# Kernel optimization log

Hardware: AMD Instinct MI355X
Metric: run time of the kernel (lower is better)

## Reference

```python
import jax, jax.numpy as jnp
import numpy as np

D_MODEL = 1024
N_HEADS = 16
D_K = D_MODEL // N_HEADS
D_FF = 4096
B, S = 2, 2048
LN_EPS = 1e-5
NEG_INF = -1e30  # finite stand-in for -inf; first (all-masked) row is overwritten by zeros anyway


def layer_norm(x, g, b):
    mu = jnp.mean(x, axis=-1, keepdims=True)
    var = jnp.mean(jnp.square(x - mu), axis=-1, keepdims=True)
    return (x - mu) * jax.lax.rsqrt(var + LN_EPS) * g + b


def setup_inputs() -> dict:
    key = jax.random.key(0)
    ks = jax.random.split(key, 16)
    sd = 0.02
    inp = {
        "query": jax.random.normal(ks[0], (B, S, D_MODEL), jnp.float32),
        "key": jax.random.normal(ks[1], (B, S, D_MODEL), jnp.float32),
        "values": jax.random.normal(ks[2], (B, S, D_MODEL), jnp.float32),
        "Wq": jax.random.normal(ks[3], (D_MODEL, D_MODEL), jnp.float32) * sd,
        "bq": jnp.zeros((D_MODEL,), jnp.float32),
        "Wk": jax.random.normal(ks[4], (D_MODEL, D_MODEL), jnp.float32) * sd,
        "bk": jnp.zeros((D_MODEL,), jnp.float32),
        "Wv": jax.random.normal(ks[5], (D_MODEL, D_MODEL), jnp.float32) * sd,
        "bv": jnp.zeros((D_MODEL,), jnp.float32),
        "Wo": jax.random.normal(ks[6], (D_MODEL, D_MODEL), jnp.float32) * sd,
        "bo": jnp.zeros((D_MODEL,), jnp.float32),
        "ln1_g": jnp.ones((D_MODEL,), jnp.float32),
        "ln1_b": jnp.zeros((D_MODEL,), jnp.float32),
        "W1": jax.random.normal(ks[7], (D_MODEL, D_FF), jnp.float32) * sd,
        "b1": jnp.zeros((D_FF,), jnp.float32),
        "W2": jax.random.normal(ks[8], (D_FF, D_MODEL), jnp.float32) * sd,
        "b2": jnp.zeros((D_MODEL,), jnp.float32),
        "ln2_g": jnp.ones((D_MODEL,), jnp.float32),
        "ln2_b": jnp.zeros((D_MODEL,), jnp.float32),
        "mask": 0,
    }
    return inp


def reference(query, key, values, Wq, bq, Wk, bk, Wv, bv, Wo, bo,
              ln1_g, ln1_b, W1, b1, W2, b2, ln2_g, ln2_b, mask):
    b, s, d = query.shape
    # projections -> [B, H, S, d_k]
    q = (query @ Wq + bq).reshape(b, s, N_HEADS, D_K).transpose(0, 2, 1, 3)
    k = (key @ Wk + bk).reshape(b, s, N_HEADS, D_K).transpose(0, 2, 1, 3)
    v = (values @ Wv + bv).reshape(b, s, N_HEADS, D_K).transpose(0, 2, 1, 3)
    # scores [B, H, S, S]
    scores = jnp.einsum("bhqd,bhkd->bhqk", q, k) / jnp.sqrt(jnp.float32(D_K))
    # torch: triu(ones, k=mask)==0 -> allowed iff j < i + mask
    i = jnp.arange(s)[:, None]
    j = jnp.arange(s)[None, :]
    allowed = j < (i + mask)
    scores = jnp.where(allowed, scores, NEG_INF)
    attn = jax.nn.softmax(scores, axis=-1)
    if mask == 0:
        # zero-pad trick: first query row (fully masked) is replaced by zeros
        attn = attn.at[:, :, 0, :].set(0.0)
    ctx = jnp.einsum("bhqk,bhkd->bhqd", attn, v)
    ctx = ctx.transpose(0, 2, 1, 3).reshape(b, s, d)
    attn_out = ctx @ Wo + bo
    x = layer_norm(query + attn_out, ln1_g, ln1_b)
    ffn = jax.nn.relu(x @ W1 + b1) @ W2 + b2
    out = layer_norm(x + ffn, ln2_g, ln2_b)
    return out
```

## Files before the change

kernel.cpp:

```cpp
#include <hip/hip_runtime.h>


typedef __attribute__((ext_vector_type(8))) __bf16 bf16x8;
typedef __attribute__((ext_vector_type(4))) float f32x4;

struct alignas(8)  S4 { short x, y, z, w; };
struct alignas(16) F4 { float x, y, z, w; };
struct alignas(16) I4 { int x, y, z, w; };

static __device__ __forceinline__ short f2bf(float f) {
  unsigned u = __float_as_uint(f);
  u += 0x7fff + ((u >> 16) & 1);
  return (short)(u >> 16);
}

static __device__ __forceinline__ void store_out(float* p, float v) { *p = v; }
static __device__ __forceinline__ void store_out(short* p, float v) { *p = f2bf(v); }

#define GLL16(g, l)                                                         \
  __builtin_amdgcn_global_load_lds(                                         \
      (__attribute__((address_space(1))) void*)(g),                         \
      (__attribute__((address_space(3))) void*)(l), 16, 0, 0)

__global__ __launch_bounds__(256) void cvt_bf16_kernel(
    const float* __restrict__ i0, const float* __restrict__ i1,
    const float* __restrict__ i2, short* __restrict__ o0,
    short* __restrict__ o1, short* __restrict__ o2) {
  int z = blockIdx.y;
  const float* in = z == 0 ? i0 : (z == 1 ? i1 : i2);
  short* out = z == 0 ? o0 : (z == 1 ? o1 : o2);
  int i = (blockIdx.x * 256 + threadIdx.x) * 4;
  F4 v = *(const F4*)(in + i);
  S4 o = { f2bf(v.x), f2bf(v.y), f2bf(v.z), f2bf(v.w) };
  *(S4*)(out + i) = o;
}

__global__ __launch_bounds__(256) void transpose_cvt_kernel(
    const float* __restrict__ Wq, const float* __restrict__ Wk,
    const float* __restrict__ Wv, const float* __restrict__ Wo,
    const float* __restrict__ W1, const float* __restrict__ W2,
    short* __restrict__ Wqt, short* __restrict__ Wkt,
    short* __restrict__ Wvt, short* __restrict__ Wot,
    short* __restrict__ W1t, short* __restrict__ W2t) {
  __shared__ float tile[64][65];
  int bid = blockIdx.x;
  const float* W; short* Wt; int K, N, kx, ny;
  if (bid < 1024) {
    int w = bid >> 8, t = bid & 255;
    W = w == 0 ? Wq : (w == 1 ? Wk : (w == 2 ? Wv : Wo));
    Wt = w == 0 ? Wqt : (w == 1 ? Wkt : (w == 2 ? Wvt : Wot));
    K = 1024; N = 1024; kx = t & 15; ny = t >> 4;
  } else if (bid < 2048) {
    int t = bid - 1024;
    W = W1; Wt = W1t; K = 1024; N = 4096; kx = t & 15; ny = t >> 4;
  } else {
    int t = bid - 2048;
    W = W2; Wt = W2t; K = 4096; N = 1024; kx = t & 63; ny = t >> 6;
  }
  int k0 = kx * 64, n0 = ny * 64;
  int tid = threadIdx.x;
  int rr = tid >> 4, cc = (tid & 15) * 4;
#pragma unroll
  for (int p = 0; p < 4; ++p) {
    int row = p * 16 + rr;
    F4 v = *(const F4*)&W[(long)(k0 + row) * N + n0 + cc];
    tile[row][cc] = v.x; tile[row][cc + 1] = v.y;
    tile[row][cc + 2] = v.z; tile[row][cc + 3] = v.w;
  }
  __syncthreads();
#pragma unroll
  for (int p = 0; p < 4; ++p) {
    int rn = p * 16 + rr;
    S4 o = { f2bf(tile[cc + 0][rn]), f2bf(tile[cc + 1][rn]),
             f2bf(tile[cc + 2][rn]), f2bf(tile[cc + 3][rn]) };
    *(S4*)&Wt[(long)(n0 + rn) * K + k0 + cc] = o;
  }
}

template <int OUT_MODE, bool RELU, bool RES, typename OT>
__device__ __forceinline__ void gemm_core(
    const short* __restrict__ A, const short* __restrict__ Bt,
    const float* __restrict__ bias, const float* __restrict__ res,
    OT* __restrict__ out, int M, int N, int K) {
  __shared__ __align__(16) short sA[128 * 64];
  __shared__ __align__(16) short sB[128 * 64];
  int tid = threadIdx.x;
  int lane = tid & 63, wave = tid >> 6;
  int col = lane & 15, quad = lane >> 4;
  int m0 = blockIdx.x * 128, n0 = blockIdx.y * 128;
  int wm = (wave & 1) * 64, wn = (wave >> 1) * 64;

  f32x4 acc[4][4] = {};

  for (int k0 = 0; k0 < K; k0 += 64) {
    __syncthreads();
#pragma unroll
    for (int j = 0; j < 4; ++j) {
      int idx = j * 256 + tid;
      int row = idx >> 3, cp = idx & 7;
      int c = cp ^ (row & 7);
      const short* ga = A  + (long)(m0 + row) * K + k0 + c * 8;
      const short* gb = Bt + (long)(n0 + row) * K + k0 + c * 8;
      short* la = &sA[(j * 256 + (wave << 6)) * 8];
      short* lb = &sB[(j * 256 + (wave << 6)) * 8];
      GLL16(ga, la);
      GLL16(gb, lb);
    }
    __syncthreads();

#pragma unroll
    for (int kk = 0; kk < 2; ++kk) {
      bf16x8 a[4], b[4];
#pragma unroll
      for (int t = 0; t < 4; ++t) {
        int ra = wm + t * 16 + col;
        int ca = kk * 4 + quad;
        a[t] = *(const bf16x8*)&sA[ra * 64 + ((ca ^ (ra & 7)) << 3)];
        int rb = wn + t * 16 + col;
        b[t] = *(const bf16x8*)&sB[rb * 64 + ((ca ^ (rb & 7)) << 3)];
      }
#pragma unroll
      for (int t = 0; t < 4; ++t)
#pragma unroll
        for (int u = 0; u < 4; ++u)
          acc[t][u] = __builtin_amdgcn_mfma_f32_16x16x32_bf16(
              a[t], b[u], acc[t][u], 0, 0, 0);
    }
  }

#pragma unroll
  for (int t = 0; t < 4; ++t) {
#pragma unroll
    for (int u = 0; u < 4; ++u) {
      int Cc = n0 + wn + u * 16 + col;
      float bv = bias[Cc];
#pragma unroll
      for (int r = 0; r < 4; ++r) {
        int R = m0 + wm + t * 16 + quad * 4 + r;
        float v = acc[t][u][r] + bv;
        if (RES) v += res[(long)R * N + Cc];
        if (RELU) v = v > 0.f ? v : 0.f;
        if (OUT_MODE == 0) {
          store_out(&out[(long)R * N + Cc], v);
        } else {
          int bb = R >> 11, s = R & 2047, h = Cc >> 6, d = Cc & 63;
          store_out(&out[((long)((bb * 16 + h) * 2048 + s) << 6) + d], v);
        }
      }
    }
  }
}

template <int OUT_MODE, bool RELU, bool RES, typename OT>
__global__ __launch_bounds__(256) void gemm_bt(
    const short* __restrict__ A, const short* __restrict__ Bt,
    const float* __restrict__ bias, const float* __restrict__ res,
    OT* __restrict__ out, int M, int N, int K) {
  gemm_core<OUT_MODE, RELU, RES, OT>(A, Bt, bias, res, out, M, N, K);
}

__global__ __launch_bounds__(256) void gemm_qkv(
    const short* __restrict__ Aq, const short* __restrict__ Ak,
    const short* __restrict__ Av, const short* __restrict__ Btq,
    const short* __restrict__ Btk, const short* __restrict__ Btv,
    const float* __restrict__ bq, const float* __restrict__ bk,
    const float* __restrict__ bv, short* __restrict__ Qp,
    short* __restrict__ Kp, short* __restrict__ Vp) {
  int z = blockIdx.z;
  const short* A = z == 0 ? Aq : (z == 1 ? Ak : Av);
  const short* Bt = z == 0 ? Btq : (z == 1 ? Btk : Btv);
  const float* bias = z == 0 ? bq : (z == 1 ? bk : bv);
  short* out = z == 0 ? Qp : (z == 1 ? Kp : Vp);
  gemm_core<1, false, false, short>(A, Bt, bias, nullptr, out, 4096, 1024, 1024);
}

__global__ __launch_bounds__(256) void attn_kernel(
    const short* __restrict__ Q, const short* __restrict__ K,
    const short* __restrict__ V, const int* __restrict__ maskp,
    float* __restrict__ pO0, float* __restrict__ pO1,
    float* __restrict__ pl) {
  __shared__ __align__(16) short sK[64 * 64];
  __shared__ __align__(16) int   sVt[64 * 32];
  __shared__ __align__(16) short sP[4 * 16 * 72];
  int tid = threadIdx.x, lane = tid & 63, wave = tid >> 6;
  int col = lane & 15, quad = lane >> 4;
  int qt = blockIdx.x, bh = blockIdx.y, chunk = blockIdx.z;
  int maskv = maskp[0];
  const long base = (long)bh * (2048 * 64);
  int i0 = qt * 64 + wave * 16;

  long jmax = (long)qt * 64 + 63 + maskv - 1;
  int tot = (jmax < 0) ? 0 : (int)(jmax >> 6) + 1;
  if (tot > 32) tot = 32;
  int half = (tot + 1) >> 1;
  int ktb = chunk ? half : 0;
  int kte = chunk ? tot : half;

  bf16x8 aQ[2];
#pragma unroll
  for (int kk = 0; kk < 2; ++kk)
    aQ[kk] = *(const bf16x8*)&Q[base + (long)(i0 + col) * 64 + kk * 32 + quad * 8];

  f32x4 o[4] = {};
  float lsum[4] = { 0.f, 0.f, 0.f, 0.f };

  int kp = tid & 31, dg = tid >> 5, d0v = dg * 8;

  for (int kt = ktb; kt < kte; ++kt) {
    __syncthreads();
#pragma unroll
    for (int j = 0; j < 2; ++j) {
      int idx = j * 256 + tid;
      int row = idx >> 3, cp = idx & 7;
      int c = cp ^ (row & 7);
      GLL16(K + base + (long)(kt * 64 + row) * 64 + c * 8,
            &sK[(j * 256 + (wave << 6)) * 8]);
    }
    {
      union { I4 v; short s[8]; } u0, u1;
      u0.v = *(const I4*)&V[base + (long)(kt * 64 + 2 * kp) * 64 + d0v];
      u1.v = *(const I4*)&V[base + (long)(kt * 64 + 2 * kp + 1) * 64 + d0v];
#pragma unroll
      for (int j = 0; j < 8; ++j) {
        int d = d0v + j;
        int w = ((int)(unsigned short)u1.s[j] << 16) | (unsigned short)u0.s[j];
        sVt[d * 32 + ((((kp >> 2) ^ (d & 7)) << 2) | (kp & 3))] = w;
      }
    }
    __syncthreads();

    f32x4 sc[4] = {};
#pragma unroll
    for (int kk = 0; kk < 2; ++kk) {
      int ca = kk * 4 + quad;
#pragma unroll
      for (int nt = 0; nt < 4; ++nt) {
        int rk = nt * 16 + col;
        bf16x8 bK = *(const bf16x8*)&sK[rk * 64 + ((ca ^ (rk & 7)) << 3)];
        sc[nt] = __builtin_amdgcn_mfma_f32_16x16x32_bf16(aQ[kk], bK, sc[nt], 0, 0, 0);
      }
    }

#pragma unroll
    for (int r = 0; r < 4; ++r) {
      int i = i0 + quad * 4 + r;
      int qr = quad * 4 + r;
#pragma unroll
      for (int nt = 0; nt < 4; ++nt) {
        int j = kt * 64 + nt * 16 + col;
        float p = (j < i + maskv) ? __expf(sc[nt][r] * 0.125f) : 0.f;
        lsum[r] += p;
        sP[wave * 1152 + qr * 72 + nt * 16 + col] = f2bf(p);
      }
    }

#pragma unroll
    for (int kk = 0; kk < 2; ++kk) {
      int ca = kk * 4 + quad;
      bf16x8 aP = *(const bf16x8*)&sP[wave * 1152 + col * 72 + ca * 8];
#pragma unroll
      for (int dt = 0; dt < 4; ++dt) {
        int d = dt * 16 + col;
        bf16x8 bV = *(const bf16x8*)((const short*)sVt + d * 64 + ((ca ^ (d & 7)) << 3));
        o[dt] = __builtin_amdgcn_mfma_f32_16x16x32_bf16(aP, bV, o[dt], 0, 0, 0);
      }
    }
  }

#pragma unroll
  for (int r = 0; r < 4; ++r)
#pragma unroll
    for (int off = 1; off < 16; off <<= 1)
      lsum[r] += __shfl_xor(lsum[r], off);

  float* pO = chunk ? pO1 : pO0;
#pragma unroll
  for (int r = 0; r < 4; ++r) {
    long row = (long)bh * 2048 + i0 + quad * 4 + r;
#pragma unroll
    for (int dt = 0; dt < 4; ++dt)
      pO[row * 64 + dt * 16 + col] = o[dt][r];
    if (col == 0) pl[((long)chunk << 16) + row] = lsum[r];
  }
}

__global__ __launch_bounds__(256) void attn_combine_kernel(
    const float* __restrict__ pO0, const float* __restrict__ pO1,
    const float* __restrict__ pl, const int* __restrict__ maskp,
    short* __restrict__ ctx) {
  int tid = threadIdx.x;
  long row = (long)blockIdx.x * 32 + (tid >> 3);
  int d0 = (tid & 7) * 8;
  float l = pl[row] + pl[row + 65536];
  float inv = (l > 0.f) ? 1.f / l : 0.f;
  int s = (int)(row & 2047);
  if (maskp[0] == 0 && s == 0) inv = 0.f;
  int bh = (int)(row >> 11), b = bh >> 4, h = bh & 15;
  F4 a0 = *(const F4*)&pO0[row * 64 + d0];
  F4 a1 = *(const F4*)&pO0[row * 64 + d0 + 4];
  F4 b0 = *(const F4*)&pO1[row * 64 + d0];
  F4 b1 = *(const F4*)&pO1[row * 64 + d0 + 4];
  S4 o0 = { f2bf((a0.x + b0.x) * inv), f2bf((a0.y + b0.y) * inv),
            f2bf((a0.z + b0.z) * inv), f2bf((a0.w + b0.w) * inv) };
  S4 o1 = { f2bf((a1.x + b1.x) * inv), f2bf((a1.y + b1.y) * inv),
            f2bf((a1.z + b1.z) * inv), f2bf((a1.w + b1.w) * inv) };
  short* dst = &ctx[((long)(b * 2048 + s)) * 1024 + h * 64 + d0];
  *(S4*)dst = o0;
  *(S4*)(dst + 4) = o1;
}

__global__ __launch_bounds__(256) void ln_kernel(
    const float* __restrict__ in, const float* __restrict__ g,
    const float* __restrict__ b, float* __restrict__ outf,
    short* __restrict__ outb) {
  int r = blockIdx.x, tid = threadIdx.x;
  int lane = tid & 63, wave = tid >> 6;
  F4 v = ((const F4*)(in + (long)r * 1024))[tid];
  float s = v.x + v.y + v.z + v.w;
  float sq = v.x * v.x + v.y * v.y + v.z * v.z + v.w * v.w;
#pragma unroll
  for (int off = 1; off < 64; off <<= 1) {
    s += __shfl_xor(s, off);
    sq += __shfl_xor(sq, off);
  }
  __shared__ float rs[4], rq[4];
  if (lane == 0) { rs[wave] = s; rq[wave] = sq; }
  __syncthreads();
  s = rs[0] + rs[1] + rs[2] + rs[3];
  sq = rq[0] + rq[1] + rq[2] + rq[3];
  float mu = s * (1.0f / 1024.0f);
  float var = sq * (1.0f / 1024.0f) - mu * mu;
  float rstd = rsqrtf(var + 1e-5f);
  F4 gv = ((const F4*)g)[tid], bv = ((const F4*)b)[tid];
  F4 o;
  o.x = (v.x - mu) * rstd * gv.x + bv.x;
  o.y = (v.y - mu) * rstd * gv.y + bv.y;
  o.z = (v.z - mu) * rstd * gv.z + bv.z;
  o.w = (v.w - mu) * rstd * gv.w + bv.w;
  ((F4*)(outf + (long)r * 1024))[tid] = o;
  if (outb) {
    S4 ob = { f2bf(o.x), f2bf(o.y), f2bf(o.z), f2bf(o.w) };
    ((S4*)(outb + (long)r * 1024))[tid] = ob;
  }
}

extern "C" void kernel_launch(void* const* d_in, const int* in_sizes, int n_in,
                              void* d_out, int out_size, void* d_ws, size_t ws_size,
                              hipStream_t stream) {
  const float* query  = (const float*)d_in[0];
  const float* keyi   = (const float*)d_in[1];
  const float* values = (const float*)d_in[2];
  const float* Wq = (const float*)d_in[3];
  const float* bq = (const float*)d_in[4];
  const float* Wk = (const float*)d_in[5];
  const float* bk = (const float*)d_in[6];
  const float* Wv = (const float*)d_in[7];
  const float* bv = (const float*)d_in[8];
  const float* Wo = (const float*)d_in[9];
  const float* bo = (const float*)d_in[10];
  const float* ln1_g = (const float*)d_in[11];
  const float* ln1_b = (const float*)d_in[12];
  const float* W1 = (const float*)d_in[13];
  const float* b1 = (const float*)d_in[14];
  const float* W2 = (const float*)d_in[15];
  const float* b2 = (const float*)d_in[16];
  const float* ln2_g = (const float*)d_in[17];
  const float* ln2_b = (const float*)d_in[18];
  const int*   maskp = (const int*)d_in[19];
  float* out = (float*)d_out;

  char* ws = (char*)d_ws;
  const size_t MB = 1u << 20;
  short* q_bf = (short*)(ws + 0);
  short* k_bf = (short*)(ws + 8 * MB);
  short* v_bf = (short*)(ws + 16 * MB);
  short* ctx  = (short*)(ws + 24 * MB);
  short* Qp   = (short*)(ws + 32 * MB);
  short* Kp   = (short*)(ws + 40 * MB);
  short* Vp   = (short*)(ws + 48 * MB);
  float* attn_res = (float*)(ws + 0);
  float* ffn_res  = (float*)(ws + 16 * MB);
  float* x_f32    = (float*)(ws + 32 * MB);
  short* x_bf     = (short*)(ws + 48 * MB);
  short* Wqt = (short*)(ws + 56 * MB);
  short* Wkt = (short*)(ws + 58 * MB);
  short* Wvt = (short*)(ws + 60 * MB);
  short* Wot = (short*)(ws + 62 * MB);
  short* W1t = (short*)(ws + 64 * MB);
  short* W2t = (short*)(ws + 72 * MB);
  short* hbuf = (short*)(ws + 80 * MB);
  float* pO0 = (float*)(ws + 0);
  float* pO1 = (float*)(ws + 80 * MB);
  float* pl  = (float*)(ws + 97 * MB);

  cvt_bf16_kernel<<<dim3(4096, 3), 256, 0, stream>>>(query, keyi, values,
                                                     q_bf, k_bf, v_bf);
  transpose_cvt_kernel<<<3072, 256, 0, stream>>>(Wq, Wk, Wv, Wo, W1, W2,
                                                 Wqt, Wkt, Wvt, Wot, W1t, W2t);
  gemm_qkv<<<dim3(32, 8, 3), 256, 0, stream>>>(q_bf, k_bf, v_bf,
                                               Wqt, Wkt, Wvt,
                                               bq, bk, bv, Qp, Kp, Vp);
  attn_kernel<<<dim3(32, 32, 2), 256, 0, stream>>>(Qp, Kp, Vp, maskp,
                                                   pO0, pO1, pl);
  attn_combine_kernel<<<2048, 256, 0, stream>>>(pO0, pO1, pl, maskp, ctx);
  gemm_bt<0, false, true, float><<<dim3(32, 8), 256, 0, stream>>>(
      ctx, Wot, bo, query, attn_res, 4096, 1024, 1024);
  ln_kernel<<<4096, 256, 0, stream>>>(attn_res, ln1_g, ln1_b, x_f32, x_bf);
  gemm_bt<0, true, false, short><<<dim3(32, 32), 256, 0, stream>>>(
      x_bf, W1t, b1, nullptr, hbuf, 4096, 4096, 1024);
  gemm_bt<0, false, true, float><<<dim3(32, 8), 256, 0, stream>>>(
      hbuf, W2t, b2, x_f32, ffn_res, 4096, 1024, 4096);
  ln_kernel<<<4096, 256, 0, stream>>>(ffn_res, ln2_g, ln2_b, out, nullptr);

  (void)in_sizes; (void)n_in; (void)out_size; (void)ws_size;
}
```

Before: 447.6 us.

## Fuse attention split-K combine, pair causal tiles, and double-buffer K/V loads

Drops the two-chunk KV split and its separate combine kernel. Each block now handles a pair of query tiles (qt and 31-qt), which balances causal work, and writes normalized bf16 ctx directly. K/V tiles are double-buffered so the next tile's loads overlap the current tile's MFMAs, with one barrier per iteration. The sP buffer gets an XOR swizzle, and a mask-free fast path handles interior tiles. The trade-off is a grid of 512 blocks instead of 2048, which lowers parallelism and occupancy, while the LDS footprint doubles.

```diff
diff --git a/kernel.cpp b/kernel.cpp
--- a/kernel.cpp
+++ b/kernel.cpp
@@ -177,136 +177,160 @@
 __global__ __launch_bounds__(256) void attn_kernel(
     const short* __restrict__ Q, const short* __restrict__ K,
     const short* __restrict__ V, const int* __restrict__ maskp,
-    float* __restrict__ pO0, float* __restrict__ pO1,
-    float* __restrict__ pl) {
-  __shared__ __align__(16) short sK[64 * 64];
-  __shared__ __align__(16) int   sVt[64 * 32];
-  __shared__ __align__(16) short sP[4 * 16 * 72];
+    short* __restrict__ ctx) {
+  __shared__ __align__(16) short sK[2][64 * 64];
+  __shared__ __align__(16) int   sVt[2][64 * 32];
+  __shared__ __align__(16) short sP[4 * 16 * 64];
   int tid = threadIdx.x, lane = tid & 63, wave = tid >> 6;
   int col = lane & 15, quad = lane >> 4;
-  int qt = blockIdx.x, bh = blockIdx.y, chunk = blockIdx.z;
+  int pair = blockIdx.x, bh = blockIdx.y;
   int maskv = maskp[0];
   const long base = (long)bh * (2048 * 64);
-  int i0 = qt * 64 + wave * 16;
-
-  long jmax = (long)qt * 64 + 63 + maskv - 1;
-  int tot = (jmax < 0) ? 0 : (int)(jmax >> 6) + 1;
-  if (tot > 32) tot = 32;
-  int half = (tot + 1) >> 1;
-  int ktb = chunk ? half : 0;
-  int kte = chunk ? tot : half;
-
-  bf16x8 aQ[2];
-#pragma unroll
-  for (int kk = 0; kk < 2; ++kk)
-    aQ[kk] = *(const bf16x8*)&Q[base + (long)(i0 + col) * 64 + kk * 32 + quad * 8];
-
-  f32x4 o[4] = {};
-  float lsum[4] = { 0.f, 0.f, 0.f, 0.f };
+  int b = bh >> 4, h = bh & 15;
 
   int kp = tid & 31, dg = tid >> 5, d0v = dg * 8;
 
-  for (int kt = ktb; kt < kte; ++kt) {
+  for (int pass = 0; pass < 2; ++pass) {
+    int qt = pass ? (31 - pair) : pair;
+    int i0 = qt * 64 + wave * 16;
+
+    long jmax = (long)qt * 64 + 63 + maskv - 1;
+    int tot = (jmax < 0) ? 0 : (int)(jmax >> 6) + 1;
+    if (tot > 32) tot = 32;
+
+    bf16x8 aQ[2];
+#pragma unroll
+    for (int kk = 0; kk < 2; ++kk)
+      aQ[kk] = *(const bf16x8*)&Q[base + (long)(i0 + col) * 64 + kk * 32 + quad * 8];
+
+    f32x4 o[4] = {};
+    float lsum[4] = { 0.f, 0.f, 0.f, 0.f };
+
+    if (tot > 0) {
+#pragma unroll
+      for (int j = 0; j < 2; ++j) {
+        int idx = j * 256 + tid;
+        int row = idx >> 3, cp = idx & 7;
+        int c = cp ^ (row & 7);
+        GLL16(K + base + (long)row * 64 + c * 8,
+              &sK[0][(j * 256 + (wave << 6)) * 8]);
+      }
+      {
+        union { I4 v; short s[8]; } u0, u1;
+        u0.v = *(const I4*)&V[base + (long)(2 * kp) * 64 + d0v];
+        u1.v = *(const I4*)&V[base + (long)(2 * kp + 1) * 64 + d0v];
+#pragma unroll
+        for (int j = 0; j < 8; ++j) {
+          int d = d0v + j;
+          int w = ((int)(unsigned short)u1.s[j] << 16) | (unsigned short)u0.s[j];
+          sVt[0][d * 32 + ((((kp >> 2) ^ (d & 7)) << 2) | (kp & 3))] = w;
+        }
+      }
+    }
     __syncthreads();
-#pragma unroll
-    for (int j = 0; j < 2; ++j) {
-      int idx = j * 256 + tid;
-      int row = idx >> 3, cp = idx & 7;
-      int c = cp ^ (row & 7);
-      GLL16(K + base + (long)(kt * 64 + row) * 64 + c * 8,
-            &sK[(j * 256 + (wave << 6)) * 8]);
-    }
-    {
+
+    for (int kt = 0; kt < tot; ++kt) {
+      int cur = kt & 1, nxt = cur ^ 1;
+      bool pf = (kt + 1 < tot);
+
       union { I4 v; short s[8]; } u0, u1;
-      u0.v = *(const I4*)&V[base + (long)(kt * 64 + 2 * kp) * 64 + d0v];
-      u1.v = *(const I4*)&V[base + (long)(kt * 64 + 2 * kp + 1) * 64 + d0v];
-#pragma unroll
-      for (int j = 0; j < 8; ++j) {
-        int d = d0v + j;
-        int w = ((int)(unsigned short)u1.s[j] << 16) | (unsigned short)u0.s[j];
-        sVt[d * 32 + ((((kp >> 2) ^ (d & 7)) << 2) | (kp & 3))] = w;
-      }
-    }
-    __syncthreads();
-
-    f32x4 sc[4] = {};
-#pragma unroll
-    for (int kk = 0; kk < 2; ++kk) {
-      int ca = kk * 4 + quad;
-#pragma unroll
-      for (int nt = 0; nt < 4; ++nt) {
-        int rk = nt * 16 + col;
-        bf16x8 bK = *(const bf16x8*)&sK[rk * 64 + ((ca ^ (rk & 7)) << 3)];
-        sc[nt] = __builtin_amdgcn_mfma_f32_16x16x32_bf16(aQ[kk], bK, sc[nt], 0, 0, 0);
-      }
-    }
+      if (pf) {
+#pragma unroll
+        for (int j = 0; j < 2; ++j) {
+          int idx = j * 256 + tid;
+          int row = idx >> 3, cp = idx & 7;
+          int c = cp ^ (row & 7);
+          GLL16(K + base + (long)((kt + 1) * 64 + row) * 64 + c * 8,
+                &sK[nxt][(j * 256 + (wave << 6)) * 8]);
+        }
+        u0.v = *(const I4*)&V[base + (long)((kt + 1) * 64 + 2 * kp) * 64 + d0v];
+        u1.v = *(const I4*)&V[base + (long)((kt + 1) * 64 + 2 * kp + 1) * 64 + d0v];
+      }
+
+      f32x4 sc[4] = {};
+#pragma unroll
+      for (int kk = 0; kk < 2; ++kk) {
+        int ca = kk * 4 + quad;
+#pragma unroll
+        for (int nt = 0; nt < 4; ++nt) {
+          int rk = nt * 16 + col;
+          bf16x8 bK = *(const bf16x8*)&sK[cur][rk * 64 + ((ca ^ (rk & 7)) << 3)];
+          sc[nt] = __builtin_amdgcn_mfma_f32_16x16x32_bf16(aQ[kk], bK, sc[nt], 0, 0, 0);
+        }
+      }
+
+      bool interior = (kt * 64 + 63) < (qt * 64 + maskv);
+      if (interior) {
+#pragma unroll
+        for (int r = 0; r < 4; ++r) {
+          int qr = quad * 4 + r;
+#pragma unroll
+          for (int nt = 0; nt < 4; ++nt) {
+            float p = __expf(sc[nt][r] * 0.125f);
+            lsum[r] += p;
+            int k8 = nt * 2 + (col >> 3);
+            sP[wave * 1024 + qr * 64 + (((k8 ^ (qr & 7)) << 3) | (col & 7))] =
+                f2bf(p);
+          }
+        }
+      } else {
+#pragma unroll
+        for (int r = 0; r < 4; ++r) {
+          int i = i0 + quad * 4 + r;
+          int qr = quad * 4 + r;
+#pragma unroll
+          for (int nt = 0; nt < 4; ++nt) {
+            int j = kt * 64 + nt * 16 + col;
+            float p = (j < i + maskv) ? __expf(sc[nt][r] * 0.125f) : 0.f;
+            lsum[r] += p;
+            int k8 = nt * 2 + (col >> 3);
+            sP[wave * 1024 + qr * 64 + (((k8 ^ (qr & 7)) << 3) | (col & 7))] =
+                f2bf(p);
+          }
+        }
+      }
+
+#pragma unroll
+      for (int kk = 0; kk < 2; ++kk) {
+        int ca = kk * 4 + quad;
+        bf16x8 aP = *(const bf16x8*)&sP[wave * 1024 + col * 64 + ((ca ^ (col & 7)) << 3)];
+#pragma unroll
+        for (int dt = 0; dt < 4; ++dt) {
+          int d = dt * 16 + col;
+          bf16x8 bV = *(const bf16x8*)((const short*)sVt[cur] + d * 64 + ((ca ^ (d & 7)) << 3));
+          o[dt] = __builtin_amdgcn_mfma_f32_16x16x32_bf16(aP, bV, o[dt], 0, 0, 0);
+        }
+      }
+
+      if (pf) {
+#pragma unroll
+        for (int j = 0; j < 8; ++j) {
+          int d = d0v + j;
+          int w = ((int)(unsigned short)u1.s[j] << 16) | (unsigned short)u0.s[j];
+          sVt[nxt][d * 32 + ((((kp >> 2) ^ (d & 7)) << 2) | (kp & 3))] = w;
+        }
+      }
+      __syncthreads();
+    }
+
+#pragma unroll
+    for (int r = 0; r < 4; ++r)
+#pragma unroll
+      for (int off = 1; off < 16; off <<= 1)
+        lsum[r] += __shfl_xor(lsum[r], off);
 
 #pragma unroll
     for (int r = 0; r < 4; ++r) {
       int i = i0 + quad * 4 + r;
-      int qr = quad * 4 + r;
-#pragma unroll
-      for (int nt = 0; nt < 4; ++nt) {
-        int j = kt * 64 + nt * 16 + col;
-        float p = (j < i + maskv) ? __expf(sc[nt][r] * 0.125f) : 0.f;
-        lsum[r] += p;
-        sP[wave * 1152 + qr * 72 + nt * 16 + col] = f2bf(p);
-      }
-    }
-
-#pragma unroll
-    for (int kk = 0; kk < 2; ++kk) {
-      int ca = kk * 4 + quad;
-      bf16x8 aP = *(const bf16x8*)&sP[wave * 1152 + col * 72 + ca * 8];
-#pragma unroll
-      for (int dt = 0; dt < 4; ++dt) {
-        int d = dt * 16 + col;
-        bf16x8 bV = *(const bf16x8*)((const short*)sVt + d * 64 + ((ca ^ (d & 7)) << 3));
-        o[dt] = __builtin_amdgcn_mfma_f32_16x16x32_bf16(aP, bV, o[dt], 0, 0, 0);
-      }
-    }
-  }
-
-#pragma unroll
-  for (int r = 0; r < 4; ++r)
-#pragma unroll
-    for (int off = 1; off < 16; off <<= 1)
-      lsum[r] += __shfl_xor(lsum[r], off);
-
-  float* pO = chunk ? pO1 : pO0;
-#pragma unroll
-  for (int r = 0; r < 4; ++r) {
-    long row = (long)bh * 2048 + i0 + quad * 4 + r;
-#pragma unroll
-    for (int dt = 0; dt < 4; ++dt)
-      pO[row * 64 + dt * 16 + col] = o[dt][r];
-    if (col == 0) pl[((long)chunk << 16) + row] = lsum[r];
-  }
-}
-
-__global__ __launch_bounds__(256) void attn_combine_kernel(
-    const float* __restrict__ pO0, const float* __restrict__ pO1,
-    const float* __restrict__ pl, const int* __restrict__ maskp,
-    short* __restrict__ ctx) {
-  int tid = threadIdx.x;
-  long row = (long)blockIdx.x * 32 + (tid >> 3);
-  int d0 = (tid & 7) * 8;
-  float l = pl[row] + pl[row + 65536];
-  float inv = (l > 0.f) ? 1.f / l : 0.f;
-  int s = (int)(row & 2047);
-  if (maskp[0] == 0 && s == 0) inv = 0.f;
-  int bh = (int)(row >> 11), b = bh >> 4, h = bh & 15;
-  F4 a0 = *(const F4*)&pO0[row * 64 + d0];
-  F4 a1 = *(const F4*)&pO0[row * 64 + d0 + 4];
-  F4 b0 = *(const F4*)&pO1[row * 64 + d0];
-  F4 b1 = *(const F4*)&pO1[row * 64 + d0 + 4];
-  S4 o0 = { f2bf((a0.x + b0.x) * inv), f2bf((a0.y + b0.y) * inv),
-            f2bf((a0.z + b0.z) * inv), f2bf((a0.w + b0.w) * inv) };
-  S4 o1 = { f2bf((a1.x + b1.x) * inv), f2bf((a1.y + b1.y) * inv),
-            f2bf((a1.z + b1.z) * inv), f2bf((a1.w + b1.w) * inv) };
-  short* dst = &ctx[((long)(b * 2048 + s)) * 1024 + h * 64 + d0];
-  *(S4*)dst = o0;
-  *(S4*)(dst + 4) = o1;
+      float inv = (lsum[r] > 0.f) ? 1.f / lsum[r] : 0.f;
+      if (maskv == 0 && i == 0) inv = 0.f;
+#pragma unroll
+      for (int dt = 0; dt < 4; ++dt)
+        ctx[(long)(b * 2048 + i) * 1024 + h * 64 + dt * 16 + col] =
+            f2bf(o[dt][r] * inv);
+    }
+    __syncthreads();
+  }
 }
 
 __global__ __launch_bounds__(256) void ln_kernel(
@@ -389,9 +413,6 @@
   short* W1t = (short*)(ws + 64 * MB);
   short* W2t = (short*)(ws + 72 * MB);
   short* hbuf = (short*)(ws + 80 * MB);
-  float* pO0 = (float*)(ws + 0);
-  float* pO1 = (float*)(ws + 80 * MB);
-  float* pl  = (float*)(ws + 97 * MB);
 
   cvt_bf16_kernel<<<dim3(4096, 3), 256, 0, stream>>>(query, keyi, values,
                                                      q_bf, k_bf, v_bf);
@@ -400,9 +421,7 @@
   gemm_qkv<<<dim3(32, 8, 3), 256, 0, stream>>>(q_bf, k_bf, v_bf,
                                                Wqt, Wkt, Wvt,
                                                bq, bk, bv, Qp, Kp, Vp);
-  attn_kernel<<<dim3(32, 32, 2), 256, 0, stream>>>(Qp, Kp, Vp, maskp,
-                                                   pO0, pO1, pl);
-  attn_combine_kernel<<<2048, 256, 0, stream>>>(pO0, pO1, pl, maskp, ctx);
+  attn_kernel<<<dim3(16, 32), 256, 0, stream>>>(Qp, Kp, Vp, maskp, ctx);
   gemm_bt<0, false, true, float><<<dim3(32, 8), 256, 0, stream>>>(
       ctx, Wot, bo, query, attn_res, 4096, 1024, 1024);
   ln_kernel<<<4096, 256, 0, stream>>>(attn_res, ln1_g, ln1_b, x_f32, x_bf);
```

Measured after the change: 422.9 us. 1.06x faster.
